# Optimization experiments

Hardware: AMD Instinct MI355X
Metric: run time of the kernel (lower is better)

## Reference

```python
import jax, jax.numpy as jnp
import numpy as np

DIM = 1024
N_HEADS = 16
HEAD_DIM = DIM // N_HEADS
BATCH = 2
SEQ = 2048


def rotate_half(x):
    x1, x2 = jnp.split(x, 2, axis=-1)
    return jnp.concatenate((-x2, x1), axis=-1)


def rope_cos_sin(seq_len, head_dim, dtype=jnp.float32):
    inv_freq = 1.0 / (10000.0 ** (jnp.arange(0, head_dim, 2, dtype=jnp.float32) / head_dim))
    t = jnp.arange(seq_len, dtype=jnp.float32)
    freqs = jnp.einsum('i,j->ij', t, inv_freq)          # [S, hd/2]
    emb = jnp.concatenate((freqs, freqs), axis=-1)       # [S, hd]
    return emb.astype(dtype)[None, :, None, :]           # [1, S, 1, hd] (cos/sin applied below)


def setup_inputs() -> dict:
    key = jax.random.key(0)
    k_x, k_q, k_k, k_v, k_o = jax.random.split(key, 5)
    scale = 1.0 / np.sqrt(DIM)
    x = jax.random.normal(k_x, (BATCH, SEQ, DIM), dtype=jnp.float32)
    Wq = jax.random.normal(k_q, (DIM, DIM), dtype=jnp.float32) * scale
    Wk = jax.random.normal(k_k, (DIM, DIM), dtype=jnp.float32) * scale
    Wv = jax.random.normal(k_v, (DIM, DIM), dtype=jnp.float32) * scale
    Wo = jax.random.normal(k_o, (DIM, DIM), dtype=jnp.float32) * scale
    # causal mask: scores masked where mask == 0
    mask = jnp.tril(jnp.ones((SEQ, SEQ), dtype=jnp.int32))[None, None, :, :]
    return {"x": x, "Wq": Wq, "Wk": Wk, "Wv": Wv, "Wo": Wo, "mask": mask}


def reference(x, Wq, Wk, Wv, Wo, mask):
    B, S, _ = x.shape
    # torch nn.Linear: y = x @ W.T
    q = (x @ Wq.T).reshape(B, S, N_HEADS, HEAD_DIM)
    k = (x @ Wk.T).reshape(B, S, N_HEADS, HEAD_DIM)
    v = (x @ Wv.T).reshape(B, S, N_HEADS, HEAD_DIM)
    ang = rope_cos_sin(S, HEAD_DIM, x.dtype)
    cos, sin = jnp.cos(ang), jnp.sin(ang)
    q = q * cos + rotate_half(q) * sin
    k = k * cos + rotate_half(k) * sin
    # [B, H, S, hd]
    q = q.transpose(0, 2, 1, 3)
    k = k.transpose(0, 2, 1, 3)
    v = v.transpose(0, 2, 1, 3)
    scores = jnp.einsum('bhqd,bhkd->bhqk', q, k) / np.sqrt(HEAD_DIM)
    scores = jnp.where(mask == 0, jnp.asarray(-1e9, scores.dtype), scores)
    attn = jax.nn.softmax(scores, axis=-1)
    out = jnp.einsum('bhqk,bhkd->bhqd', attn, v)
    out = out.transpose(0, 2, 1, 3).reshape(B, S, DIM)
    return out @ Wo.T
```

## Files before the change

### kernel.cpp

```cpp
#include <hip/hip_runtime.h>
#include <stdint.h>

typedef unsigned short u16;
typedef __bf16 bf16x8 __attribute__((ext_vector_type(8)));
typedef __bf16 bf16x4 __attribute__((ext_vector_type(4)));
typedef float f32x4 __attribute__((ext_vector_type(4)));

#define N_B 2
#define N_S 2048
#define N_D 1024
#define N_H 16
#define HD 64

#if __has_builtin(__builtin_amdgcn_exp2f)
#define EXP2F(x) __builtin_amdgcn_exp2f(x)
#else
#define EXP2F(x) exp2f(x)
#endif

__device__ __forceinline__ u16 f2bf(float f) {
  union { float f; uint32_t u; } v; v.f = f;
  uint32_t u = v.u + 0x7fffu + ((v.u >> 16) & 1u);
  return (u16)(u >> 16);
}

__device__ __forceinline__ void gload16(const u16* g, u16* lds) {
  __builtin_amdgcn_global_load_lds(
      (const __attribute__((address_space(1))) unsigned int*)g,
      (__attribute__((address_space(3))) unsigned int*)lds, 16, 0, 0);
}

__global__ __launch_bounds__(256) void prep_kernel(
    const float* __restrict__ x, const float* __restrict__ Wq,
    const float* __restrict__ Wk, const float* __restrict__ Wv,
    const float* __restrict__ Wo,
    u16* __restrict__ xb, u16* __restrict__ wqb, u16* __restrict__ wkb,
    u16* __restrict__ wvb, u16* __restrict__ wob,
    float* __restrict__ cosT, float* __restrict__ sinT)
{
  const int NX = N_B * N_S * N_D;
  const int NW = N_D * N_D;
  int bid = blockIdx.x;
  if (bid < 8192) {
    int i = (bid * 256 + threadIdx.x) * 4;
    const float* src; u16* dst; int off;
    if (i < NX) { src = x; dst = xb; off = i; }
    else {
      int j = i - NX;
      int w = j >> 20;
      off = j & (NW - 1);
      src = (w == 0) ? Wq : (w == 1) ? Wk : (w == 2) ? Wv : Wo;
      dst = (w == 0) ? wqb : (w == 1) ? wkb : (w == 2) ? wvb : wob;
    }
    float4 v = *(const float4*)(src + off);
    ushort4 o;
    o.x = f2bf(v.x); o.y = f2bf(v.y); o.z = f2bf(v.z); o.w = f2bf(v.w);
    *(ushort4*)(dst + off) = o;
  } else {
    int t = (bid - 8192) * 256 + threadIdx.x;
    int s = t >> 5, i = t & 31;
    float inv = expf(-(float)i * 0.28782313662425574f);
    float a = (float)s * inv;
    float sn, cs;
    sincosf(a, &sn, &cs);
    cosT[t] = cs;
    sinT[t] = sn;
  }
}

__global__ __launch_bounds__(256) void proj_kernel(
    const u16* __restrict__ x, const u16* __restrict__ Wq,
    const u16* __restrict__ Wk, const u16* __restrict__ Wv,
    u16* __restrict__ Qb, u16* __restrict__ Kb, u16* __restrict__ Vtb,
    const float* __restrict__ cosT, const float* __restrict__ sinT)
{
  const int mode = blockIdx.z;
  const u16* Wm = (mode == 0) ? Wq : (mode == 1) ? Wk : Wv;
  const int bx = blockIdx.x, by = blockIdx.y;
  const int tid = threadIdx.x;
  const int wave = tid >> 6, lane = tid & 63;
  const int c = lane & 15, quad = lane >> 4;
  const int wm = wave & 1, wn = wave >> 1;

  __shared__ __align__(16) u16 As[128 * 32];
  __shared__ __align__(16) u16 Bs[128 * 32];

  const f32x4 zero = {0.f, 0.f, 0.f, 0.f};
  f32x4 acc[4][4];
#pragma unroll
  for (int i = 0; i < 4; ++i)
#pragma unroll
    for (int j = 0; j < 4; ++j) acc[i][j] = zero;

  for (int kt = 0; kt < 32; ++kt) {
    const int k0 = kt * 32;
    __syncthreads();
#pragma unroll
    for (int t = 0; t < 2; ++t) {
      int p = t * 256 + tid;
      int m = p >> 2, sl = p & 3;
      int kq = sl ^ ((m >> 1) & 3);
      gload16(x  + (size_t)(by * 128 + m) * N_D + k0 + kq * 8, &As[(t * 256 + wave * 64) * 8]);
      gload16(Wm + (size_t)(bx * 128 + m) * N_D + k0 + kq * 8, &Bs[(t * 256 + wave * 64) * 8]);
    }
    __syncthreads();
    bf16x8 av[4], bv[4];
#pragma unroll
    for (int i = 0; i < 4; ++i) {
      int m = wm * 64 + i * 16 + c;
      int sa = quad ^ ((m >> 1) & 3);
      av[i] = *(const bf16x8*)&As[(m * 4 + sa) * 8];
      int n = wn * 64 + i * 16 + c;
      int sb = quad ^ ((n >> 1) & 3);
      bv[i] = *(const bf16x8*)&Bs[(n * 4 + sb) * 8];
    }
#pragma unroll
    for (int i = 0; i < 4; ++i)
#pragma unroll
      for (int j = 0; j < 4; ++j)
        acc[i][j] = __builtin_amdgcn_mfma_f32_16x16x32_bf16(av[i], bv[j], acc[i][j], 0, 0, 0);
  }

  const int h = bx * 2 + wn;
  if (mode < 2) {
    u16* Out = (mode == 0) ? Qb : Kb;
#pragma unroll
    for (int i = 0; i < 4; ++i) {
#pragma unroll
      for (int r = 0; r < 4; ++r) {
        int row = by * 128 + wm * 64 + i * 16 + quad * 4 + r;
        int b = row >> 11, s = row & 2047;
        float cs0 = cosT[s * 32 + c],      sn0 = sinT[s * 32 + c];
        float cs1 = cosT[s * 32 + 16 + c], sn1 = sinT[s * 32 + 16 + c];
        size_t base = ((size_t)(b * N_H + h) * N_S + s) * HD;
#pragma unroll
        for (int j = 0; j < 4; ++j) {
          float v = acc[i][j][r];
          float p = acc[i][j ^ 2][r];
          float cs = (j & 1) ? cs1 : cs0;
          float sn = (j & 1) ? sn1 : sn0;
          float res = (j < 2) ? (v * cs - p * sn) : (v * cs + p * sn);
          Out[base + j * 16 + c] = f2bf(res);
        }
      }
    }
  } else {
#pragma unroll
    for (int i = 0; i < 4; ++i) {
      int srow = by * 128 + wm * 64 + i * 16 + quad * 4;
      int b = srow >> 11, sb = srow & 2047;
#pragma unroll
      for (int j = 0; j < 4; ++j) {
        int d = j * 16 + c;
        ushort4 pk;
        pk.x = f2bf(acc[i][j][0]);
        pk.y = f2bf(acc[i][j][1]);
        pk.z = f2bf(acc[i][j][2]);
        pk.w = f2bf(acc[i][j][3]);
        *(ushort4*)&Vtb[((size_t)(b * N_H + h) * HD + d) * N_S + sb] = pk;
      }
    }
  }
}

__global__ __launch_bounds__(64, 2) void attn_kernel(
    const u16* __restrict__ Qb, const u16* __restrict__ Kb,
    const u16* __restrict__ Vtb, u16* __restrict__ Ab)
{
  const int lane = threadIdx.x;
  const int c = lane & 15, quad = lane >> 4;
  const int bx = blockIdx.x;
  const int xcd = bx & 7;
  const int idx = bx >> 3;
  const int s = idx >> 5;
  const int r = idx & 31;
  const int bh = xcd + (r & 3) * 8;
  const int g = r >> 2;
  const int t = (s < 4) ? (63 - g - s * 8) : (g + (s - 4) * 8);
  const int q0 = t * 32;
  const int ktmax = t >> 1;
  const int maskch = t & 1;

  __shared__ __align__(16) u16 Ks[64 * 64];
  __shared__ __align__(16) u16 Vs[64 * 64];
  __shared__ __align__(16) u16 Ps[32 * 32];

  const u16* Qg = Qb + ((size_t)bh * N_S + q0) * HD;
  const u16* Kg = Kb + (size_t)bh * N_S * HD;
  const u16* Vg = Vtb + (size_t)bh * HD * N_S;

  bf16x8 qreg[2][2];
#pragma unroll
  for (int jQ = 0; jQ < 2; ++jQ)
#pragma unroll
    for (int ks = 0; ks < 2; ++ks)
      qreg[jQ][ks] = *(const bf16x8*)(Qg + (jQ * 16 + c) * HD + ks * 32 + quad * 8);

  const f32x4 zero = {0.f, 0.f, 0.f, 0.f};
  f32x4 acc_o[2][4];
#pragma unroll
  for (int mt = 0; mt < 2; ++mt)
#pragma unroll
    for (int nt = 0; nt < 4; ++nt) acc_o[mt][nt] = zero;
  float lrow[2] = {0.f, 0.f};

  const float CLOG = 0.18033688011112042f;
  const float FM = 16.0f;

  for (int kt = 0; kt <= ktmax; ++kt) {
    asm volatile("s_waitcnt lgkmcnt(0)" ::: "memory");
#pragma unroll
    for (int i = 0; i < 8; ++i) {
      int ci = i * 64 + lane;
      int m = ci >> 3, sl = ci & 7;
      int kq = sl ^ (m & 7);
      gload16(Kg + (size_t)(kt * 64 + m) * HD + kq * 8, &Ks[i * 512]);
    }
#pragma unroll
    for (int i = 0; i < 8; ++i) {
      int ci = i * 64 + lane;
      int d = ci >> 3, sl = ci & 7;
      int kq = sl ^ (d & 7);
      gload16(Vg + (size_t)d * N_S + kt * 64 + kq * 8, &Vs[i * 512]);
    }
    asm volatile("s_waitcnt vmcnt(8)" ::: "memory");

    const bool diag = (kt == ktmax);
    const int nch = (diag && maskch == 0) ? 1 : 2;

#pragma unroll
    for (int ch = 0; ch < 2; ++ch) {
      if (ch < nch) {
        f32x4 acc_s[2][2];
#pragma unroll
        for (int iK = 0; iK < 2; ++iK)
#pragma unroll
          for (int jQ = 0; jQ < 2; ++jQ) acc_s[iK][jQ] = zero;
#pragma unroll
        for (int ks = 0; ks < 2; ++ks) {
          bf16x8 kf[2];
#pragma unroll
          for (int iK = 0; iK < 2; ++iK) {
            int m = ch * 32 + iK * 16 + c;
            kf[iK] = *(const bf16x8*)&Ks[(m * 8 + (((ks * 4 + quad) ^ (c & 7)))) * 8];
          }
#pragma unroll
          for (int iK = 0; iK < 2; ++iK)
#pragma unroll
            for (int jQ = 0; jQ < 2; ++jQ)
              acc_s[iK][jQ] = __builtin_amdgcn_mfma_f32_16x16x32_bf16(
                  kf[iK], qreg[jQ][ks], acc_s[iK][jQ], 0, 0, 0);
        }

        const bool domask = diag && (ch == maskch);
#pragma unroll
        for (int iK = 0; iK < 2; ++iK)
#pragma unroll
          for (int jQ = 0; jQ < 2; ++jQ) {
            bf16x4 pb;
#pragma unroll
            for (int rr = 0; rr < 4; ++rr) {
              float arg = fmaf(acc_s[iK][jQ][rr], CLOG, -FM);
              if (domask) {
                int dsk = iK * 16 + quad * 4 + rr;
                int dq = jQ * 16 + c;
                if (dsk > dq) arg = -3.0e38f;
              }
              float p = EXP2F(arg);
              lrow[jQ] += p;
              pb[rr] = (__bf16)p;
            }
            int q = jQ * 16 + c;
            int slot = (iK * 2 + (quad >> 1)) ^ (q & 3);
            *(bf16x4*)&Ps[q * 32 + slot * 8 + (quad & 1) * 4] = pb;
          }

        if (ch == 0) asm volatile("s_waitcnt vmcnt(0)" ::: "memory");

        bf16x8 pf[2], vf[4];
#pragma unroll
        for (int nt = 0; nt < 4; ++nt) {
          int d = nt * 16 + c;
          vf[nt] = *(const bf16x8*)&Vs[(d * 8 + (((ch * 4 + quad) ^ (d & 7)))) * 8];
        }
#pragma unroll
        for (int mt = 0; mt < 2; ++mt) {
          int q = mt * 16 + c;
          pf[mt] = *(const bf16x8*)&Ps[q * 32 + ((quad ^ (q & 3)) * 8)];
        }
#pragma unroll
        for (int mt = 0; mt < 2; ++mt)
#pragma unroll
          for (int nt = 0; nt < 4; ++nt)
            acc_o[mt][nt] = __builtin_amdgcn_mfma_f32_16x16x32_bf16(
                pf[mt], vf[nt], acc_o[mt][nt], 0, 0, 0);
      }
    }
  }

#pragma unroll
  for (int jQ = 0; jQ < 2; ++jQ) {
    float l = lrow[jQ];
    l += __shfl_xor(l, 16, 64);
    l += __shfl_xor(l, 32, 64);
    lrow[jQ] = 1.0f / l;
  }
  const int b = bh >> 4, h = bh & 15;
#pragma unroll
  for (int mt = 0; mt < 2; ++mt) {
#pragma unroll
    for (int rr = 0; rr < 4; ++rr) {
      float inv = __shfl(lrow[mt], quad * 4 + rr, 64);
      int q = q0 + mt * 16 + quad * 4 + rr;
#pragma unroll
      for (int nt = 0; nt < 4; ++nt) {
        Ab[((size_t)(b * N_S + q)) * N_D + h * HD + nt * 16 + c] =
            f2bf(acc_o[mt][nt][rr] * inv);
      }
    }
  }
}

__global__ __launch_bounds__(256) void out_gemm_kernel(
    const u16* __restrict__ A, const u16* __restrict__ Wo, float* __restrict__ out)
{
  const int bx = blockIdx.x, by = blockIdx.y;
  const int tid = threadIdx.x;
  const int wave = tid >> 6, lane = tid & 63;
  const int c = lane & 15, quad = lane >> 4;
  const int wn = wave;

  __shared__ __align__(16) u16 As[64 * 32];
  __shared__ __align__(16) u16 Bs[128 * 32];

  const f32x4 zero = {0.f, 0.f, 0.f, 0.f};
  f32x4 acc[4][2];
#pragma unroll
  for (int i = 0; i < 4; ++i)
#pragma unroll
    for (int j = 0; j < 2; ++j) acc[i][j] = zero;

  for (int kt = 0; kt < 32; ++kt) {
    const int k0 = kt * 32;
    __syncthreads();
    {
      int m = tid >> 2, sl = tid & 3;
      int kq = sl ^ ((m >> 1) & 3);
      gload16(A + (size_t)(by * 64 + m) * N_D + k0 + kq * 8, &As[(wave * 64) * 8]);
    }
#pragma unroll
    for (int t = 0; t < 2; ++t) {
      int p = t * 256 + tid;
      int m = p >> 2, sl = p & 3;
      int kq = sl ^ ((m >> 1) & 3);
      gload16(Wo + (size_t)(bx * 128 + m) * N_D + k0 + kq * 8, &Bs[(t * 256 + wave * 64) * 8]);
    }
    __syncthreads();
    bf16x8 av[4], bv[2];
#pragma unroll
    for (int i = 0; i < 4; ++i) {
      int m = i * 16 + c;
      int sa = quad ^ ((m >> 1) & 3);
      av[i] = *(const bf16x8*)&As[(m * 4 + sa) * 8];
    }
#pragma unroll
    for (int j = 0; j < 2; ++j) {
      int n = wn * 32 + j * 16 + c;
      int sb = quad ^ ((n >> 1) & 3);
      bv[j] = *(const bf16x8*)&Bs[(n * 4 + sb) * 8];
    }
#pragma unroll
    for (int i = 0; i < 4; ++i)
#pragma unroll
      for (int j = 0; j < 2; ++j)
        acc[i][j] = __builtin_amdgcn_mfma_f32_16x16x32_bf16(av[i], bv[j], acc[i][j], 0, 0, 0);
  }

#pragma unroll
  for (int i = 0; i < 4; ++i)
#pragma unroll
    for (int r = 0; r < 4; ++r) {
      int row = by * 64 + i * 16 + quad * 4 + r;
#pragma unroll
      for (int j = 0; j < 2; ++j) {
        int col = bx * 128 + wn * 32 + j * 16 + c;
        out[(size_t)row * N_D + col] = acc[i][j][r];
      }
    }
}

extern "C" void kernel_launch(void* const* d_in, const int* in_sizes, int n_in,
                              void* d_out, int out_size, void* d_ws, size_t ws_size,
                              hipStream_t stream) {
  const float* x  = (const float*)d_in[0];
  const float* Wq = (const float*)d_in[1];
  const float* Wk = (const float*)d_in[2];
  const float* Wv = (const float*)d_in[3];
  const float* Wo = (const float*)d_in[4];
  float* out = (float*)d_out;
  char* ws = (char*)d_ws;
  u16* xb   = (u16*)(ws);
  u16* Wqb  = (u16*)(ws + ( 8u << 20));
  u16* Wkb  = (u16*)(ws + (10u << 20));
  u16* Wvb  = (u16*)(ws + (12u << 20));
  u16* Wob  = (u16*)(ws + (14u << 20));
  u16* Qb   = (u16*)(ws + (16u << 20));
  u16* Kb   = (u16*)(ws + (24u << 20));
  u16* Vtb  = (u16*)(ws + (32u << 20));
  u16* Ab   = (u16*)(ws + (40u << 20));
  float* cosT = (float*)(ws + (48u << 20));
  float* sinT = (float*)(ws + (48u << 20) + (1u << 20));

  prep_kernel<<<8448, 256, 0, stream>>>(x, Wq, Wk, Wv, Wo,
                                        xb, Wqb, Wkb, Wvb, Wob, cosT, sinT);
  proj_kernel<<<dim3(8, 32, 3), 256, 0, stream>>>(xb, Wqb, Wkb, Wvb, Qb, Kb, Vtb, cosT, sinT);
  attn_kernel<<<2048, 64, 0, stream>>>(Qb, Kb, Vtb, Ab);
  out_gemm_kernel<<<dim3(8, 64), 256, 0, stream>>>(Ab, Wob, out);
}
```

Baseline: 209.1 us.

## Retile projection, attention and output GEMMs with smaller tiles and deeper K steps

The QKV projection now uses 128x64 tiles with a K step of 64 and one head per block, and the output GEMM uses 64x64 tiles with a K step of 64. Both grids double in size to give more blocks and better occupancy, and both use 8-slot XOR swizzles. The attention kernel drops the 64-key chunking and reorder scheme and processes 32-key tiles with a single mask on the diagonal tile, using a simpler longest-first block order and occupancy 3. The cost is more loop iterations and barriers per attention block and less reuse per GEMM tile.

Result: no change. 207.4 us (-0.8%).

```diff
diff --git a/kernel.cpp b/kernel.cpp
--- a/kernel.cpp
+++ b/kernel.cpp
@@ -68,7 +68,7 @@
   }
 }
 
-__global__ __launch_bounds__(256) void proj_kernel(
+__global__ __launch_bounds__(256, 5) void proj_kernel(
     const u16* __restrict__ x, const u16* __restrict__ Wq,
     const u16* __restrict__ Wk, const u16* __restrict__ Wv,
     u16* __restrict__ Qb, u16* __restrict__ Kb, u16* __restrict__ Vtb,
@@ -80,55 +80,65 @@
   const int tid = threadIdx.x;
   const int wave = tid >> 6, lane = tid & 63;
   const int c = lane & 15, quad = lane >> 4;
-  const int wm = wave & 1, wn = wave >> 1;
-
-  __shared__ __align__(16) u16 As[128 * 32];
-  __shared__ __align__(16) u16 Bs[128 * 32];
+
+  __shared__ __align__(16) u16 As[128 * 64];
+  __shared__ __align__(16) u16 Bs[64 * 64];
 
   const f32x4 zero = {0.f, 0.f, 0.f, 0.f};
-  f32x4 acc[4][4];
-#pragma unroll
-  for (int i = 0; i < 4; ++i)
+  f32x4 acc[2][4];
+#pragma unroll
+  for (int i = 0; i < 2; ++i)
 #pragma unroll
     for (int j = 0; j < 4; ++j) acc[i][j] = zero;
 
-  for (int kt = 0; kt < 32; ++kt) {
-    const int k0 = kt * 32;
+  for (int kt = 0; kt < 16; ++kt) {
+    const int k0 = kt * 64;
     __syncthreads();
+#pragma unroll
+    for (int t = 0; t < 4; ++t) {
+      int p = t * 256 + tid;
+      int m = p >> 3, sl = p & 7;
+      int kq = sl ^ (m & 7);
+      gload16(x + (size_t)(by * 128 + m) * N_D + k0 + kq * 8, &As[(t * 256 + wave * 64) * 8]);
+    }
 #pragma unroll
     for (int t = 0; t < 2; ++t) {
       int p = t * 256 + tid;
-      int m = p >> 2, sl = p & 3;
-      int kq = sl ^ ((m >> 1) & 3);
-      gload16(x  + (size_t)(by * 128 + m) * N_D + k0 + kq * 8, &As[(t * 256 + wave * 64) * 8]);
-      gload16(Wm + (size_t)(bx * 128 + m) * N_D + k0 + kq * 8, &Bs[(t * 256 + wave * 64) * 8]);
+      int m = p >> 3, sl = p & 7;
+      int kq = sl ^ (m & 7);
+      gload16(Wm + (size_t)(bx * 64 + m) * N_D + k0 + kq * 8, &Bs[(t * 256 + wave * 64) * 8]);
     }
     __syncthreads();
-    bf16x8 av[4], bv[4];
-#pragma unroll
-    for (int i = 0; i < 4; ++i) {
-      int m = wm * 64 + i * 16 + c;
-      int sa = quad ^ ((m >> 1) & 3);
-      av[i] = *(const bf16x8*)&As[(m * 4 + sa) * 8];
-      int n = wn * 64 + i * 16 + c;
-      int sb = quad ^ ((n >> 1) & 3);
-      bv[i] = *(const bf16x8*)&Bs[(n * 4 + sb) * 8];
-    }
-#pragma unroll
-    for (int i = 0; i < 4; ++i)
-#pragma unroll
-      for (int j = 0; j < 4; ++j)
-        acc[i][j] = __builtin_amdgcn_mfma_f32_16x16x32_bf16(av[i], bv[j], acc[i][j], 0, 0, 0);
-  }
-
-  const int h = bx * 2 + wn;
+#pragma unroll
+    for (int ks = 0; ks < 2; ++ks) {
+      bf16x8 av[2], bv[4];
+      int kq = ks * 4 + quad;
+#pragma unroll
+      for (int i = 0; i < 2; ++i) {
+        int m = wave * 32 + i * 16 + c;
+        av[i] = *(const bf16x8*)&As[(m * 8 + (kq ^ (m & 7))) * 8];
+      }
+#pragma unroll
+      for (int j = 0; j < 4; ++j) {
+        int n = j * 16 + c;
+        bv[j] = *(const bf16x8*)&Bs[(n * 8 + (kq ^ (n & 7))) * 8];
+      }
+#pragma unroll
+      for (int i = 0; i < 2; ++i)
+#pragma unroll
+        for (int j = 0; j < 4; ++j)
+          acc[i][j] = __builtin_amdgcn_mfma_f32_16x16x32_bf16(av[i], bv[j], acc[i][j], 0, 0, 0);
+    }
+  }
+
+  const int h = bx;
   if (mode < 2) {
     u16* Out = (mode == 0) ? Qb : Kb;
 #pragma unroll
-    for (int i = 0; i < 4; ++i) {
+    for (int i = 0; i < 2; ++i) {
 #pragma unroll
       for (int r = 0; r < 4; ++r) {
-        int row = by * 128 + wm * 64 + i * 16 + quad * 4 + r;
+        int row = by * 128 + wave * 32 + i * 16 + quad * 4 + r;
         int b = row >> 11, s = row & 2047;
         float cs0 = cosT[s * 32 + c],      sn0 = sinT[s * 32 + c];
         float cs1 = cosT[s * 32 + 16 + c], sn1 = sinT[s * 32 + 16 + c];
@@ -146,8 +156,8 @@
     }
   } else {
 #pragma unroll
-    for (int i = 0; i < 4; ++i) {
-      int srow = by * 128 + wm * 64 + i * 16 + quad * 4;
+    for (int i = 0; i < 2; ++i) {
+      int srow = by * 128 + wave * 32 + i * 16 + quad * 4;
       int b = srow >> 11, sb = srow & 2047;
 #pragma unroll
       for (int j = 0; j < 4; ++j) {
@@ -163,7 +173,7 @@
   }
 }
 
-__global__ __launch_bounds__(64, 2) void attn_kernel(
+__global__ __launch_bounds__(64, 3) void attn_kernel(
     const u16* __restrict__ Qb, const u16* __restrict__ Kb,
     const u16* __restrict__ Vtb, u16* __restrict__ Ab)
 {
@@ -172,17 +182,13 @@
   const int bx = blockIdx.x;
   const int xcd = bx & 7;
   const int idx = bx >> 3;
-  const int s = idx >> 5;
-  const int r = idx & 31;
-  const int bh = xcd + (r & 3) * 8;
-  const int g = r >> 2;
-  const int t = (s < 4) ? (63 - g - s * 8) : (g + (s - 4) * 8);
+  const int t = 63 - (idx >> 2);
+  const int bh = xcd + (idx & 3) * 8;
   const int q0 = t * 32;
-  const int ktmax = t >> 1;
-  const int maskch = t & 1;
-
-  __shared__ __align__(16) u16 Ks[64 * 64];
-  __shared__ __align__(16) u16 Vs[64 * 64];
+  const int ktmax = t;
+
+  __shared__ __align__(16) u16 Ks[32 * 64];
+  __shared__ __align__(16) u16 Vs[64 * 32];
   __shared__ __align__(16) u16 Ps[32 * 32];
 
   const u16* Qg = Qb + ((size_t)bh * N_S + q0) * HD;
@@ -210,92 +216,85 @@
   for (int kt = 0; kt <= ktmax; ++kt) {
     asm volatile("s_waitcnt lgkmcnt(0)" ::: "memory");
 #pragma unroll
-    for (int i = 0; i < 8; ++i) {
+    for (int i = 0; i < 4; ++i) {
       int ci = i * 64 + lane;
       int m = ci >> 3, sl = ci & 7;
       int kq = sl ^ (m & 7);
-      gload16(Kg + (size_t)(kt * 64 + m) * HD + kq * 8, &Ks[i * 512]);
-    }
-#pragma unroll
-    for (int i = 0; i < 8; ++i) {
+      gload16(Kg + (size_t)(kt * 32 + m) * HD + kq * 8, &Ks[i * 512]);
+    }
+#pragma unroll
+    for (int i = 0; i < 4; ++i) {
       int ci = i * 64 + lane;
-      int d = ci >> 3, sl = ci & 7;
-      int kq = sl ^ (d & 7);
-      gload16(Vg + (size_t)d * N_S + kt * 64 + kq * 8, &Vs[i * 512]);
-    }
-    asm volatile("s_waitcnt vmcnt(8)" ::: "memory");
-
-    const bool diag = (kt == ktmax);
-    const int nch = (diag && maskch == 0) ? 1 : 2;
-
-#pragma unroll
-    for (int ch = 0; ch < 2; ++ch) {
-      if (ch < nch) {
-        f32x4 acc_s[2][2];
-#pragma unroll
-        for (int iK = 0; iK < 2; ++iK)
-#pragma unroll
-          for (int jQ = 0; jQ < 2; ++jQ) acc_s[iK][jQ] = zero;
-#pragma unroll
-        for (int ks = 0; ks < 2; ++ks) {
-          bf16x8 kf[2];
-#pragma unroll
-          for (int iK = 0; iK < 2; ++iK) {
-            int m = ch * 32 + iK * 16 + c;
-            kf[iK] = *(const bf16x8*)&Ks[(m * 8 + (((ks * 4 + quad) ^ (c & 7)))) * 8];
+      int d = ci >> 2, sl = ci & 3;
+      int kq = sl ^ (d & 3);
+      gload16(Vg + (size_t)d * N_S + kt * 32 + kq * 8, &Vs[i * 512]);
+    }
+    asm volatile("s_waitcnt vmcnt(4)" ::: "memory");
+
+    f32x4 acc_s[2][2];
+#pragma unroll
+    for (int iK = 0; iK < 2; ++iK)
+#pragma unroll
+      for (int jQ = 0; jQ < 2; ++jQ) acc_s[iK][jQ] = zero;
+#pragma unroll
+    for (int ks = 0; ks < 2; ++ks) {
+      bf16x8 kf[2];
+      int kq = ks * 4 + quad;
+#pragma unroll
+      for (int iK = 0; iK < 2; ++iK) {
+        int m = iK * 16 + c;
+        kf[iK] = *(const bf16x8*)&Ks[(m * 8 + (kq ^ (m & 7))) * 8];
+      }
+#pragma unroll
+      for (int iK = 0; iK < 2; ++iK)
+#pragma unroll
+        for (int jQ = 0; jQ < 2; ++jQ)
+          acc_s[iK][jQ] = __builtin_amdgcn_mfma_f32_16x16x32_bf16(
+              kf[iK], qreg[jQ][ks], acc_s[iK][jQ], 0, 0, 0);
+    }
+
+    const bool domask = (kt == ktmax);
+#pragma unroll
+    for (int iK = 0; iK < 2; ++iK)
+#pragma unroll
+      for (int jQ = 0; jQ < 2; ++jQ) {
+        bf16x4 pb;
+#pragma unroll
+        for (int rr = 0; rr < 4; ++rr) {
+          float arg = fmaf(acc_s[iK][jQ][rr], CLOG, -FM);
+          if (domask) {
+            int dsk = iK * 16 + quad * 4 + rr;
+            int dq = jQ * 16 + c;
+            if (dsk > dq) arg = -3.0e38f;
           }
-#pragma unroll
-          for (int iK = 0; iK < 2; ++iK)
-#pragma unroll
-            for (int jQ = 0; jQ < 2; ++jQ)
-              acc_s[iK][jQ] = __builtin_amdgcn_mfma_f32_16x16x32_bf16(
-                  kf[iK], qreg[jQ][ks], acc_s[iK][jQ], 0, 0, 0);
+          float p = EXP2F(arg);
+          lrow[jQ] += p;
+          pb[rr] = (__bf16)p;
         }
-
-        const bool domask = diag && (ch == maskch);
-#pragma unroll
-        for (int iK = 0; iK < 2; ++iK)
-#pragma unroll
-          for (int jQ = 0; jQ < 2; ++jQ) {
-            bf16x4 pb;
-#pragma unroll
-            for (int rr = 0; rr < 4; ++rr) {
-              float arg = fmaf(acc_s[iK][jQ][rr], CLOG, -FM);
-              if (domask) {
-                int dsk = iK * 16 + quad * 4 + rr;
-                int dq = jQ * 16 + c;
-                if (dsk > dq) arg = -3.0e38f;
-              }
-              float p = EXP2F(arg);
-              lrow[jQ] += p;
-              pb[rr] = (__bf16)p;
-            }
-            int q = jQ * 16 + c;
-            int slot = (iK * 2 + (quad >> 1)) ^ (q & 3);
-            *(bf16x4*)&Ps[q * 32 + slot * 8 + (quad & 1) * 4] = pb;
-          }
-
-        if (ch == 0) asm volatile("s_waitcnt vmcnt(0)" ::: "memory");
-
-        bf16x8 pf[2], vf[4];
-#pragma unroll
-        for (int nt = 0; nt < 4; ++nt) {
-          int d = nt * 16 + c;
-          vf[nt] = *(const bf16x8*)&Vs[(d * 8 + (((ch * 4 + quad) ^ (d & 7)))) * 8];
-        }
-#pragma unroll
-        for (int mt = 0; mt < 2; ++mt) {
-          int q = mt * 16 + c;
-          pf[mt] = *(const bf16x8*)&Ps[q * 32 + ((quad ^ (q & 3)) * 8)];
-        }
-#pragma unroll
-        for (int mt = 0; mt < 2; ++mt)
-#pragma unroll
-          for (int nt = 0; nt < 4; ++nt)
-            acc_o[mt][nt] = __builtin_amdgcn_mfma_f32_16x16x32_bf16(
-                pf[mt], vf[nt], acc_o[mt][nt], 0, 0, 0);
-      }
-    }
+        int q = jQ * 16 + c;
+        int slot = (iK * 2 + (quad >> 1)) ^ (q & 3);
+        *(bf16x4*)&Ps[q * 32 + slot * 8 + (quad & 1) * 4] = pb;
+      }
+
+    asm volatile("s_waitcnt vmcnt(0)" ::: "memory");
+
+    bf16x8 pf[2], vf[4];
+#pragma unroll
+    for (int nt = 0; nt < 4; ++nt) {
+      int d = nt * 16 + c;
+      vf[nt] = *(const bf16x8*)&Vs[(d * 4 + (quad ^ (d & 3))) * 8];
+    }
+#pragma unroll
+    for (int mt = 0; mt < 2; ++mt) {
+      int q = mt * 16 + c;
+      pf[mt] = *(const bf16x8*)&Ps[q * 32 + ((quad ^ (q & 3)) * 8)];
+    }
+#pragma unroll
+    for (int mt = 0; mt < 2; ++mt)
+#pragma unroll
+      for (int nt = 0; nt < 4; ++nt)
+        acc_o[mt][nt] = __builtin_amdgcn_mfma_f32_16x16x32_bf16(
+            pf[mt], vf[nt], acc_o[mt][nt], 0, 0, 0);
   }
 
 #pragma unroll
@@ -328,62 +327,66 @@
   const int tid = threadIdx.x;
   const int wave = tid >> 6, lane = tid & 63;
   const int c = lane & 15, quad = lane >> 4;
-  const int wn = wave;
-
-  __shared__ __align__(16) u16 As[64 * 32];
-  __shared__ __align__(16) u16 Bs[128 * 32];
+  const int wm = wave & 1, wn = wave >> 1;
+
+  __shared__ __align__(16) u16 As[64 * 64];
+  __shared__ __align__(16) u16 Bs[64 * 64];
 
   const f32x4 zero = {0.f, 0.f, 0.f, 0.f};
-  f32x4 acc[4][2];
-#pragma unroll
-  for (int i = 0; i < 4; ++i)
+  f32x4 acc[2][2];
+#pragma unroll
+  for (int i = 0; i < 2; ++i)
 #pragma unroll
     for (int j = 0; j < 2; ++j) acc[i][j] = zero;
 
-  for (int kt = 0; kt < 32; ++kt) {
-    const int k0 = kt * 32;
+  for (int kt = 0; kt < 16; ++kt) {
+    const int k0 = kt * 64;
     __syncthreads();
-    {
-      int m = tid >> 2, sl = tid & 3;
-      int kq = sl ^ ((m >> 1) & 3);
-      gload16(A + (size_t)(by * 64 + m) * N_D + k0 + kq * 8, &As[(wave * 64) * 8]);
-    }
 #pragma unroll
     for (int t = 0; t < 2; ++t) {
       int p = t * 256 + tid;
-      int m = p >> 2, sl = p & 3;
-      int kq = sl ^ ((m >> 1) & 3);
-      gload16(Wo + (size_t)(bx * 128 + m) * N_D + k0 + kq * 8, &Bs[(t * 256 + wave * 64) * 8]);
+      int m = p >> 3, sl = p & 7;
+      int kq = sl ^ (m & 7);
+      gload16(A + (size_t)(by * 64 + m) * N_D + k0 + kq * 8, &As[(t * 256 + wave * 64) * 8]);
+    }
+#pragma unroll
+    for (int t = 0; t < 2; ++t) {
+      int p = t * 256 + tid;
+      int m = p >> 3, sl = p & 7;
+      int kq = sl ^ (m & 7);
+      gload16(Wo + (size_t)(bx * 64 + m) * N_D + k0 + kq * 8, &Bs[(t * 256 + wave * 64) * 8]);
     }
     __syncthreads();
-    bf16x8 av[4], bv[2];
-#pragma unroll
-    for (int i = 0; i < 4; ++i) {
-      int m = i * 16 + c;
-      int sa = quad ^ ((m >> 1) & 3);
-      av[i] = *(const bf16x8*)&As[(m * 4 + sa) * 8];
-    }
-#pragma unroll
-    for (int j = 0; j < 2; ++j) {
-      int n = wn * 32 + j * 16 + c;
-      int sb = quad ^ ((n >> 1) & 3);
-      bv[j] = *(const bf16x8*)&Bs[(n * 4 + sb) * 8];
-    }
-#pragma unroll
-    for (int i = 0; i < 4; ++i)
-#pragma unroll
-      for (int j = 0; j < 2; ++j)
-        acc[i][j] = __builtin_amdgcn_mfma_f32_16x16x32_bf16(av[i], bv[j], acc[i][j], 0, 0, 0);
-  }
-
-#pragma unroll
-  for (int i = 0; i < 4; ++i)
+#pragma unroll
+    for (int ks = 0; ks < 2; ++ks) {
+      bf16x8 av[2], bv[2];
+      int kq = ks * 4 + quad;
+#pragma unroll
+      for (int i = 0; i < 2; ++i) {
+        int m = wm * 32 + i * 16 + c;
+        av[i] = *(const bf16x8*)&As[(m * 8 + (kq ^ (m & 7))) * 8];
+      }
+#pragma unroll
+      for (int j = 0; j < 2; ++j) {
+        int n = wn * 32 + j * 16 + c;
+        bv[j] = *(const bf16x8*)&Bs[(n * 8 + (kq ^ (n & 7))) * 8];
+      }
+#pragma unroll
+      for (int i = 0; i < 2; ++i)
+#pragma unroll
+        for (int j = 0; j < 2; ++j)
+          acc[i][j] = __builtin_amdgcn_mfma_f32_16x16x32_bf16(av[i], bv[j], acc[i][j], 0, 0, 0);
+    }
+  }
+
+#pragma unroll
+  for (int i = 0; i < 2; ++i)
 #pragma unroll
     for (int r = 0; r < 4; ++r) {
-      int row = by * 64 + i * 16 + quad * 4 + r;
+      int row = by * 64 + wm * 32 + i * 16 + quad * 4 + r;
 #pragma unroll
       for (int j = 0; j < 2; ++j) {
-        int col = bx * 128 + wn * 32 + j * 16 + c;
+        int col = bx * 64 + wn * 32 + j * 16 + c;
         out[(size_t)row * N_D + col] = acc[i][j][r];
       }
     }
@@ -413,7 +416,7 @@
 
   prep_kernel<<<8448, 256, 0, stream>>>(x, Wq, Wk, Wv, Wo,
                                         xb, Wqb, Wkb, Wvb, Wob, cosT, sinT);
-  proj_kernel<<<dim3(8, 32, 3), 256, 0, stream>>>(xb, Wqb, Wkb, Wvb, Qb, Kb, Vtb, cosT, sinT);
+  proj_kernel<<<dim3(16, 32, 3), 256, 0, stream>>>(xb, Wqb, Wkb, Wvb, Qb, Kb, Vtb, cosT, sinT);
   attn_kernel<<<2048, 64, 0, stream>>>(Qb, Kb, Vtb, Ab);
-  out_gemm_kernel<<<dim3(8, 64), 256, 0, stream>>>(Ab, Wob, out);
-}
+  out_gemm_kernel<<<dim3(16, 64), 256, 0, stream>>>(Ab, Wob, out);
+}
```
